# Kernel optimization log

Measured on AMD Instinct MI355X. Metric: run time of the kernel, lower is better.

Reference implementation:

```python
import jax, jax.numpy as jnp
import numpy as np

N = 100000   # nodes
E = 1600000  # edges
H = 128      # num_features == hidden_size
C = 64       # num_classes
BN_EPS = 1e-5


def setup_inputs() -> dict:
    key = jax.random.key(0)
    ks = jax.random.split(key, 11)
    return {
        "x": jax.random.normal(ks[0], (N, H), jnp.float32),
        "edge_index": jax.random.randint(ks[1], (2, E), 0, N, dtype=jnp.int32),
        "edge_attr": jax.random.normal(ks[2], (E,), jnp.float32),
        "conv_w": jax.random.normal(ks[3], (2, 3, H, H), jnp.float32) / np.sqrt(H).astype(np.float32),
        "conv_b": jax.random.normal(ks[4], (2, 3, H), jnp.float32) * 0.1,
        "bn_g": jax.random.uniform(ks[5], (2, 3, H), jnp.float32, 0.5, 1.5),
        "bn_b": jax.random.normal(ks[6], (2, 3, H), jnp.float32) * 0.1,
        "bn_m": jax.random.normal(ks[7], (2, 3, H), jnp.float32) * 0.1,
        "bn_v": jax.random.uniform(ks[8], (2, 3, H), jnp.float32, 0.5, 1.5),
        "fc_w": jax.random.normal(ks[9], (H, C), jnp.float32) / np.sqrt(H).astype(np.float32),
        "fc_b": jax.random.normal(ks[10], (C,), jnp.float32) * 0.1,
    }


def _gin_conv(h, edge_index, w, b, g, beta, m, v):
    # GIN: out = MLP((1+eps)*x + sum_{j in N(i)} x_j), eps=0 (PyG default)
    src, dst = edge_index[0], edge_index[1]
    agg = jax.ops.segment_sum(h[src], dst, num_segments=N)  # [N,H] scatter-add
    h = h + agg
    for i in range(3):  # Linear -> BatchNorm1d (eval stats) -> ReLU
        h = h @ w[i] + b[i]
        h = (h - m[i]) * jax.lax.rsqrt(v[i] + BN_EPS) * g[i] + beta[i]
        h = jax.nn.relu(h)
    return h


def reference(x, edge_index, edge_attr, conv_w, conv_b, bn_g, bn_b, bn_m, bn_v, fc_w, fc_b):
    # edge_attr is ignored by default PyG GINConv (no edge weighting in GIN)
    h = jax.nn.relu(_gin_conv(x, edge_index, conv_w[0], conv_b[0], bn_g[0], bn_b[0], bn_m[0], bn_v[0]))
    h = jax.nn.relu(_gin_conv(h, edge_index, conv_w[1], conv_b[1], bn_g[1], bn_b[1], bn_m[1], bn_v[1]))
    # dropout is identity in eval mode
    logits = h @ fc_w + fc_b  # [N,C]
    return jax.nn.log_softmax(logits, axis=1)
```

## Files before the change

### kernel.cpp

```cpp
#include <hip/hip_runtime.h>

#define NN 100000
#define NE 1600000
#define HF 128
#define NC 64
#define AP 136
#define NB 196
#define BSH 9
#define BMASK 511
#define BCAP 9216

typedef __bf16 bf16x8 __attribute__((ext_vector_type(8)));
typedef float  f32x4  __attribute__((ext_vector_type(4)));
typedef unsigned short us8 __attribute__((ext_vector_type(8)));

__device__ __forceinline__ unsigned short f2b(float x) {
  unsigned int u = __float_as_uint(x);
  u += 0x7FFFu + ((u >> 16) & 1u);
  return (unsigned short)(u >> 16);
}
__device__ __forceinline__ float b2f(unsigned short b) {
  return __uint_as_float(((unsigned int)b) << 16);
}

__global__ void prep_weights(const float* __restrict__ conv_w, const float* __restrict__ conv_b,
                             const float* __restrict__ bn_g, const float* __restrict__ bn_b,
                             const float* __restrict__ bn_m, const float* __restrict__ bn_v,
                             const float* __restrict__ fc_w,
                             unsigned short* __restrict__ wt, unsigned short* __restrict__ wtf,
                             float* __restrict__ sarr, float* __restrict__ tarr) {
  int idx = blockIdx.x * 256 + threadIdx.x;
  if (idx < 6 * HF * HF) {
    int j  = idx & 7;
    int m  = (idx >> 3) & 15;
    int q  = (idx >> 7) & 3;
    int nt = (idx >> 9) & 7;
    int k0 = (idx >> 12) & 3;
    int ls = idx >> 14;
    int k = k0 * 32 + q * 8 + j;
    int n = nt * 16 + m;
    wt[idx] = f2b(conv_w[(ls * HF + k) * HF + n]);
  }
  if (idx < HF * NC) {
    int j  = idx & 7;
    int m  = (idx >> 3) & 15;
    int q  = (idx >> 7) & 3;
    int nt = (idx >> 9) & 3;
    int k0 = idx >> 11;
    int k = k0 * 32 + q * 8 + j;
    int c = nt * 16 + m;
    wtf[idx] = f2b(fc_w[k * NC + c]);
  }
  if (idx < 6 * HF) {
    float s = bn_g[idx] * rsqrtf(bn_v[idx] + 1e-5f);
    sarr[idx] = s;
    tarr[idx] = (conv_b[idx] - bn_m[idx]) * s + bn_b[idx];
  }
}

__global__ __launch_bounds__(256) void cast_bf16(const float* __restrict__ x,
                                                 unsigned short* __restrict__ xb) {
  size_t i = (size_t)(blockIdx.x * 256 + threadIdx.x) * 8;
  float4 a = *(const float4*)(x + i);
  float4 b = *(const float4*)(x + i + 4);
  us8 v = { f2b(a.x), f2b(a.y), f2b(a.z), f2b(a.w),
            f2b(b.x), f2b(b.y), f2b(b.z), f2b(b.w) };
  *(us8*)(xb + i) = v;
}

__global__ void init_gcur(int* __restrict__ gcur) {
  int t = threadIdx.x;
  if (t < NB) gcur[t] = t * BCAP;
}

__global__ __launch_bounds__(256) void bin_edges(const int* __restrict__ src,
                                                 const int* __restrict__ dst,
                                                 int* __restrict__ gcur,
                                                 unsigned int* __restrict__ binned) {
  __shared__ int hist[NB];
  int t = threadIdx.x;
  if (t < NB) hist[t] = 0;
  __syncthreads();
  int base = blockIdx.x * 8192;
  for (int j = 0; j < 32; j++) {
    int e = base + j * 256 + t;
    if (e < NE) atomicAdd(&hist[dst[e] >> BSH], 1);
  }
  __syncthreads();
  if (t < NB) {
    int c = hist[t];
    if (c) hist[t] = atomicAdd(&gcur[t], c);
  }
  __syncthreads();
  for (int j = 0; j < 32; j++) {
    int e = base + j * 256 + t;
    if (e < NE) {
      int d = dst[e];
      int b = d >> BSH;
      int p = atomicAdd(&hist[b], 1);
      binned[p] = (unsigned int)src[e] | ((unsigned int)(d & BMASK) << 17);
    }
  }
}

__global__ __launch_bounds__(256) void build_csr(const unsigned int* __restrict__ binned,
                                                 const int* __restrict__ gcur,
                                                 int* __restrict__ offs,
                                                 int* __restrict__ deg,
                                                 int* __restrict__ csr) {
  __shared__ int ncnt[512];
  __shared__ int sm[256];
  int t = threadIdx.x;
  int b = blockIdx.x;
  int beg = b * BCAP;
  int cntb = gcur[b] - beg;
  ncnt[t] = 0; ncnt[t + 256] = 0;
  __syncthreads();
  for (int e = beg + t; e < beg + cntb; e += 256) atomicAdd(&ncnt[binned[e] >> 17], 1);
  __syncthreads();
  int c0 = ncnt[2 * t], c1 = ncnt[2 * t + 1];
  int s = c0 + c1;
  sm[t] = s; __syncthreads();
  for (int off = 1; off < 256; off <<= 1) {
    int u = (t >= off) ? sm[t - off] : 0;
    __syncthreads();
    sm[t] += u;
    __syncthreads();
  }
  int ex = sm[t] - s + beg;
  int node0 = (b << BSH) + 2 * t;
  if (node0 < NN)     { offs[node0]     = ex;      deg[node0]     = c0; }
  if (node0 + 1 < NN) { offs[node0 + 1] = ex + c0; deg[node0 + 1] = c1; }
  ncnt[2 * t]     = ex;
  ncnt[2 * t + 1] = ex + c0;
  __syncthreads();
  for (int e = beg + t; e < beg + cntb; e += 256) {
    unsigned int u = binned[e];
    int p = atomicAdd(&ncnt[u >> 17], 1);
    csr[p] = (int)(u & 0x1FFFFu);
  }
}

__global__ __launch_bounds__(256) void aggregate(const unsigned short* __restrict__ h,
                                                 const int* __restrict__ offs,
                                                 const int* __restrict__ deg,
                                                 const int* __restrict__ csr,
                                                 unsigned short* __restrict__ out) {
  int wave = threadIdx.x >> 6;
  int lane = threadIdx.x & 63;
  int node = blockIdx.x * 4 + wave;
  if (node >= NN) return;
  int g  = lane >> 4;
  int sl = lane & 15;
  int beg = offs[node];
  int dg  = deg[node];

  float acc[8];
  if (g == 0) {
    us8 v = *(const us8*)(h + (size_t)node * HF + sl * 8);
    #pragma unroll
    for (int i = 0; i < 8; i++) acc[i] = b2f(v[i]);
  } else {
    #pragma unroll
    for (int i = 0; i < 8; i++) acc[i] = 0.f;
  }

  for (int e = beg + g; e < beg + dg; e += 4) {
    int s = csr[e];
    us8 v = *(const us8*)(h + (size_t)s * HF + sl * 8);
    #pragma unroll
    for (int i = 0; i < 8; i++) acc[i] += b2f(v[i]);
  }

  #pragma unroll
  for (int i = 0; i < 8; i++) {
    acc[i] += __shfl_xor(acc[i], 16, 64);
    acc[i] += __shfl_xor(acc[i], 32, 64);
  }
  if (g == 0) {
    us8 r;
    #pragma unroll
    for (int i = 0; i < 8; i++) r[i] = f2b(acc[i]);
    *(us8*)(out + (size_t)node * HF + sl * 8) = r;
  }
}

__device__ __forceinline__ void mlp3_body(const unsigned short* __restrict__ in,
                                          unsigned short* Ab,
                                          const unsigned short* __restrict__ wt,
                                          const float* __restrict__ sarr,
                                          const float* __restrict__ tarr,
                                          int layer, int row0, int wave, int lane,
                                          bf16x8 af[4]) {
  int m = lane & 15, q = lane >> 4;
  int node = row0 + wave * 16 + m;
  int nclamp = (node < NN) ? node : 0;
  #pragma unroll
  for (int k0 = 0; k0 < 4; k0++)
    af[k0] = *(const bf16x8*)(in + (size_t)nclamp * HF + k0 * 32 + q * 8);

  const unsigned short* wbase = wt + layer * 3 * 16384;
  #pragma unroll
  for (int sub = 0; sub < 3; sub++) {
    const unsigned short* wsub = wbase + sub * 16384;
    f32x4 acc[8];
    #pragma unroll
    for (int nt = 0; nt < 8; nt++) {
      acc[nt] = (f32x4){0.f, 0.f, 0.f, 0.f};
      #pragma unroll
      for (int k0 = 0; k0 < 4; k0++) {
        bf16x8 bf = *(const bf16x8*)(wsub + ((k0 * 8 + nt) * 64 + lane) * 8);
        acc[nt] = __builtin_amdgcn_mfma_f32_16x16x32_bf16(af[k0], bf, acc[nt], 0, 0, 0);
      }
    }
    const float* sp = sarr + (layer * 3 + sub) * HF;
    const float* tp = tarr + (layer * 3 + sub) * HF;
    #pragma unroll
    for (int nt = 0; nt < 8; nt++) {
      int c = nt * 16 + m;
      float sc = sp[c], sh = tp[c];
      #pragma unroll
      for (int i = 0; i < 4; i++) {
        int r = wave * 16 + q * 4 + i;
        float y = fmaxf(acc[nt][i] * sc + sh, 0.f);
        Ab[r * AP + c] = f2b(y);
      }
    }
    #pragma unroll
    for (int k0 = 0; k0 < 4; k0++)
      af[k0] = *(const bf16x8*)&Ab[(wave * 16 + m) * AP + k0 * 32 + q * 8];
  }
}

__global__ __launch_bounds__(256) void mlp3(const unsigned short* __restrict__ in,
                                            unsigned short* __restrict__ out,
                                            const unsigned short* __restrict__ wt,
                                            const float* __restrict__ sarr,
                                            const float* __restrict__ tarr) {
  __shared__ unsigned short Ab[64 * AP];
  int t = threadIdx.x;
  int lane = t & 63, wave = t >> 6;
  int row0 = blockIdx.x * 64;
  bf16x8 af[4];
  mlp3_body(in, Ab, wt, sarr, tarr, 0, row0, wave, lane, af);

  for (int it = 0; it < 4; it++) {
    int idx = it * 64 + lane;
    int r = wave * 16 + (idx >> 4);
    int c = (idx & 15) << 3;
    int gr = row0 + r;
    if (gr < NN) *(us8*)(out + (size_t)gr * HF + c) = *(const us8*)&Ab[r * AP + c];
  }
}

__global__ __launch_bounds__(256) void mlp3fc(const unsigned short* __restrict__ in,
                                              float* __restrict__ out,
                                              const unsigned short* __restrict__ wt,
                                              const float* __restrict__ sarr,
                                              const float* __restrict__ tarr,
                                              const unsigned short* __restrict__ wtf,
                                              const float* __restrict__ fc_b) {
  __shared__ unsigned short Ab[64 * AP];
  int t = threadIdx.x;
  int lane = t & 63, wave = t >> 6;
  int row0 = blockIdx.x * 64;
  int m = lane & 15, q = lane >> 4;
  bf16x8 af[4];
  mlp3_body(in, Ab, wt, sarr, tarr, 1, row0, wave, lane, af);

  f32x4 acc[4];
  #pragma unroll
  for (int nt = 0; nt < 4; nt++) {
    acc[nt] = (f32x4){0.f, 0.f, 0.f, 0.f};
    #pragma unroll
    for (int k0 = 0; k0 < 4; k0++) {
      bf16x8 bf = *(const bf16x8*)(wtf + ((k0 * 4 + nt) * 64 + lane) * 8);
      acc[nt] = __builtin_amdgcn_mfma_f32_16x16x32_bf16(af[k0], bf, acc[nt], 0, 0, 0);
    }
  }
  float v[4][4];
  #pragma unroll
  for (int nt = 0; nt < 4; nt++) {
    float b = fc_b[nt * 16 + m];
    #pragma unroll
    for (int i = 0; i < 4; i++) v[nt][i] = acc[nt][i] + b;
  }
  float mx[4], sum[4];
  #pragma unroll
  for (int i = 0; i < 4; i++) {
    mx[i] = fmaxf(fmaxf(v[0][i], v[1][i]), fmaxf(v[2][i], v[3][i]));
    mx[i] = fmaxf(mx[i], __shfl_xor(mx[i], 1, 64));
    mx[i] = fmaxf(mx[i], __shfl_xor(mx[i], 2, 64));
    mx[i] = fmaxf(mx[i], __shfl_xor(mx[i], 4, 64));
    mx[i] = fmaxf(mx[i], __shfl_xor(mx[i], 8, 64));
    sum[i] = __expf(v[0][i] - mx[i]) + __expf(v[1][i] - mx[i])
           + __expf(v[2][i] - mx[i]) + __expf(v[3][i] - mx[i]);
    sum[i] += __shfl_xor(sum[i], 1, 64);
    sum[i] += __shfl_xor(sum[i], 2, 64);
    sum[i] += __shfl_xor(sum[i], 4, 64);
    sum[i] += __shfl_xor(sum[i], 8, 64);
    sum[i] = __logf(sum[i]) + mx[i];
  }
  #pragma unroll
  for (int i = 0; i < 4; i++) {
    int gr = row0 + wave * 16 + q * 4 + i;
    if (gr < NN) {
      #pragma unroll
      for (int nt = 0; nt < 4; nt++)
        out[(size_t)gr * NC + nt * 16 + m] = v[nt][i] - sum[i];
    }
  }
}

extern "C" void kernel_launch(void* const* d_in, const int* in_sizes, int n_in,
                              void* d_out, int out_size, void* d_ws, size_t ws_size,
                              hipStream_t stream) {
  const float* x      = (const float*)d_in[0];
  const int*   ei     = (const int*)d_in[1];
  const float* conv_w = (const float*)d_in[3];
  const float* conv_b = (const float*)d_in[4];
  const float* bn_g   = (const float*)d_in[5];
  const float* bn_b   = (const float*)d_in[6];
  const float* bn_m   = (const float*)d_in[7];
  const float* bn_v   = (const float*)d_in[8];
  const float* fc_w   = (const float*)d_in[9];
  const float* fc_b   = (const float*)d_in[10];
  float* out = (float*)d_out;

  const int* srcI = ei;
  const int* dstI = ei + NE;

  unsigned short* Xb   = (unsigned short*)d_ws;
  unsigned short* Abuf = Xb + (size_t)NN * HF;
  unsigned short* Bbuf = Abuf + (size_t)NN * HF;
  int* gcur   = (int*)(Bbuf + (size_t)NN * HF);
  int* offs   = gcur + 256;
  int* deg    = offs + 100004;
  unsigned int* binned = (unsigned int*)(deg + 100004);
  int* csr    = (int*)(binned + (size_t)NB * BCAP);
  unsigned short* wt  = (unsigned short*)(csr + (size_t)NB * BCAP);
  unsigned short* wtf = wt + 6 * HF * HF;
  float* sarr = (float*)(wtf + HF * NC);
  float* tarr = sarr + 6 * HF;

  prep_weights<<<384, 256, 0, stream>>>(conv_w, conv_b, bn_g, bn_b, bn_m, bn_v, fc_w,
                                        wt, wtf, sarr, tarr);
  cast_bf16<<<6250, 256, 0, stream>>>(x, Xb);
  init_gcur<<<1, 256, 0, stream>>>(gcur);
  bin_edges<<<196, 256, 0, stream>>>(srcI, dstI, gcur, binned);
  build_csr<<<196, 256, 0, stream>>>(binned, gcur, offs, deg, csr);

  aggregate<<<NN / 4, 256, 0, stream>>>(Xb, offs, deg, csr, Abuf);
  mlp3<<<(NN + 63) / 64, 256, 0, stream>>>(Abuf, Bbuf, wt, sarr, tarr);
  aggregate<<<NN / 4, 256, 0, stream>>>(Bbuf, offs, deg, csr, Abuf);
  mlp3fc<<<(NN + 63) / 64, 256, 0, stream>>>(Abuf, out, wt, sarr, tarr, wtf, fc_b);
}
```

Measured before the change: 383.3 us.

## Fuse prologue kernels and double edge-binning bucket count with wider blocks

Merges weight prep, input bf16 cast and bucket-cursor init into a single prologue kernel to cut launches. Halves the bucket width (256 nodes per bin, 391 bins) and uses 512-thread blocks for binning and CSR build so more workgroups run in parallel across the CUs. The binning kernel also keeps src/dst in registers between its two passes instead of reloading them. More bins mean more global atomics on the cursors, and bucket capacity headroom is tighter relative to the expected edges per bin.

```diff
diff --git a/kernel.cpp b/kernel.cpp
--- a/kernel.cpp
+++ b/kernel.cpp
@@ -5,10 +5,10 @@
 #define HF 128
 #define NC 64
 #define AP 136
-#define NB 196
-#define BSH 9
-#define BMASK 511
-#define BCAP 9216
+#define NB 391
+#define BSH 8
+#define BMASK 255
+#define BCAP 4608
 
 typedef __bf16 bf16x8 __attribute__((ext_vector_type(8)));
 typedef float  f32x4  __attribute__((ext_vector_type(4)));
@@ -23,13 +23,29 @@
   return __uint_as_float(((unsigned int)b) << 16);
 }
 
-__global__ void prep_weights(const float* __restrict__ conv_w, const float* __restrict__ conv_b,
-                             const float* __restrict__ bn_g, const float* __restrict__ bn_b,
-                             const float* __restrict__ bn_m, const float* __restrict__ bn_v,
-                             const float* __restrict__ fc_w,
-                             unsigned short* __restrict__ wt, unsigned short* __restrict__ wtf,
-                             float* __restrict__ sarr, float* __restrict__ tarr) {
+__global__ __launch_bounds__(256) void prologue(const float* __restrict__ x,
+                                                unsigned short* __restrict__ xb,
+                                                const float* __restrict__ conv_w,
+                                                const float* __restrict__ conv_b,
+                                                const float* __restrict__ bn_g,
+                                                const float* __restrict__ bn_b,
+                                                const float* __restrict__ bn_m,
+                                                const float* __restrict__ bn_v,
+                                                const float* __restrict__ fc_w,
+                                                unsigned short* __restrict__ wt,
+                                                unsigned short* __restrict__ wtf,
+                                                float* __restrict__ sarr,
+                                                float* __restrict__ tarr,
+                                                int* __restrict__ gcur) {
   int idx = blockIdx.x * 256 + threadIdx.x;
+  {
+    size_t i = (size_t)idx * 8;
+    float4 a = *(const float4*)(x + i);
+    float4 b = *(const float4*)(x + i + 4);
+    us8 v = { f2b(a.x), f2b(a.y), f2b(a.z), f2b(a.w),
+              f2b(b.x), f2b(b.y), f2b(b.z), f2b(b.w) };
+    *(us8*)(xb + i) = v;
+  }
   if (idx < 6 * HF * HF) {
     int j  = idx & 7;
     int m  = (idx >> 3) & 15;
@@ -56,24 +72,10 @@
     sarr[idx] = s;
     tarr[idx] = (conv_b[idx] - bn_m[idx]) * s + bn_b[idx];
   }
-}
-
-__global__ __launch_bounds__(256) void cast_bf16(const float* __restrict__ x,
-                                                 unsigned short* __restrict__ xb) {
-  size_t i = (size_t)(blockIdx.x * 256 + threadIdx.x) * 8;
-  float4 a = *(const float4*)(x + i);
-  float4 b = *(const float4*)(x + i + 4);
-  us8 v = { f2b(a.x), f2b(a.y), f2b(a.z), f2b(a.w),
-            f2b(b.x), f2b(b.y), f2b(b.z), f2b(b.w) };
-  *(us8*)(xb + i) = v;
-}
-
-__global__ void init_gcur(int* __restrict__ gcur) {
-  int t = threadIdx.x;
-  if (t < NB) gcur[t] = t * BCAP;
-}
-
-__global__ __launch_bounds__(256) void bin_edges(const int* __restrict__ src,
+  if (idx < NB) gcur[idx] = idx * BCAP;
+}
+
+__global__ __launch_bounds__(512) void bin_edges(const int* __restrict__ src,
                                                  const int* __restrict__ dst,
                                                  int* __restrict__ gcur,
                                                  unsigned int* __restrict__ binned) {
@@ -81,10 +83,15 @@
   int t = threadIdx.x;
   if (t < NB) hist[t] = 0;
   __syncthreads();
-  int base = blockIdx.x * 8192;
-  for (int j = 0; j < 32; j++) {
-    int e = base + j * 256 + t;
-    if (e < NE) atomicAdd(&hist[dst[e] >> BSH], 1);
+  int base = blockIdx.x * 4096;
+  int sv[8], dv[8];
+  #pragma unroll
+  for (int j = 0; j < 8; j++) {
+    int e = base + j * 512 + t;
+    bool ok = e < NE;
+    dv[j] = ok ? dst[e] : -1;
+    sv[j] = ok ? src[e] : 0;
+    if (ok) atomicAdd(&hist[dv[j] >> BSH], 1);
   }
   __syncthreads();
   if (t < NB) {
@@ -92,49 +99,48 @@
     if (c) hist[t] = atomicAdd(&gcur[t], c);
   }
   __syncthreads();
-  for (int j = 0; j < 32; j++) {
-    int e = base + j * 256 + t;
-    if (e < NE) {
-      int d = dst[e];
-      int b = d >> BSH;
+  #pragma unroll
+  for (int j = 0; j < 8; j++) {
+    if (dv[j] >= 0) {
+      int b = dv[j] >> BSH;
       int p = atomicAdd(&hist[b], 1);
-      binned[p] = (unsigned int)src[e] | ((unsigned int)(d & BMASK) << 17);
-    }
-  }
-}
-
-__global__ __launch_bounds__(256) void build_csr(const unsigned int* __restrict__ binned,
+      binned[p] = (unsigned int)sv[j] | ((unsigned int)(dv[j] & BMASK) << 17);
+    }
+  }
+}
+
+__global__ __launch_bounds__(512) void build_csr(const unsigned int* __restrict__ binned,
                                                  const int* __restrict__ gcur,
                                                  int* __restrict__ offs,
                                                  int* __restrict__ deg,
                                                  int* __restrict__ csr) {
-  __shared__ int ncnt[512];
+  __shared__ int ncnt[256];
   __shared__ int sm[256];
   int t = threadIdx.x;
   int b = blockIdx.x;
   int beg = b * BCAP;
   int cntb = gcur[b] - beg;
-  ncnt[t] = 0; ncnt[t + 256] = 0;
-  __syncthreads();
-  for (int e = beg + t; e < beg + cntb; e += 256) atomicAdd(&ncnt[binned[e] >> 17], 1);
-  __syncthreads();
-  int c0 = ncnt[2 * t], c1 = ncnt[2 * t + 1];
-  int s = c0 + c1;
-  sm[t] = s; __syncthreads();
+  if (t < 256) ncnt[t] = 0;
+  __syncthreads();
+  for (int e = beg + t; e < beg + cntb; e += 512) atomicAdd(&ncnt[binned[e] >> 17], 1);
+  __syncthreads();
+  int s = 0;
+  if (t < 256) { s = ncnt[t]; sm[t] = s; }
+  __syncthreads();
   for (int off = 1; off < 256; off <<= 1) {
-    int u = (t >= off) ? sm[t - off] : 0;
+    int u = (t < 256 && t >= off) ? sm[t - off] : 0;
     __syncthreads();
-    sm[t] += u;
+    if (t < 256) sm[t] += u;
     __syncthreads();
   }
-  int ex = sm[t] - s + beg;
-  int node0 = (b << BSH) + 2 * t;
-  if (node0 < NN)     { offs[node0]     = ex;      deg[node0]     = c0; }
-  if (node0 + 1 < NN) { offs[node0 + 1] = ex + c0; deg[node0 + 1] = c1; }
-  ncnt[2 * t]     = ex;
-  ncnt[2 * t + 1] = ex + c0;
-  __syncthreads();
-  for (int e = beg + t; e < beg + cntb; e += 256) {
+  if (t < 256) {
+    int ex = sm[t] - s + beg;
+    int node = (b << BSH) + t;
+    if (node < NN) { offs[node] = ex; deg[node] = s; }
+    ncnt[t] = ex;
+  }
+  __syncthreads();
+  for (int e = beg + t; e < beg + cntb; e += 512) {
     unsigned int u = binned[e];
     int p = atomicAdd(&ncnt[u >> 17], 1);
     csr[p] = (int)(u & 0x1FFFFu);
@@ -334,7 +340,7 @@
   unsigned short* Abuf = Xb + (size_t)NN * HF;
   unsigned short* Bbuf = Abuf + (size_t)NN * HF;
   int* gcur   = (int*)(Bbuf + (size_t)NN * HF);
-  int* offs   = gcur + 256;
+  int* offs   = gcur + 512;
   int* deg    = offs + 100004;
   unsigned int* binned = (unsigned int*)(deg + 100004);
   int* csr    = (int*)(binned + (size_t)NB * BCAP);
@@ -343,12 +349,10 @@
   float* sarr = (float*)(wtf + HF * NC);
   float* tarr = sarr + 6 * HF;
 
-  prep_weights<<<384, 256, 0, stream>>>(conv_w, conv_b, bn_g, bn_b, bn_m, bn_v, fc_w,
-                                        wt, wtf, sarr, tarr);
-  cast_bf16<<<6250, 256, 0, stream>>>(x, Xb);
-  init_gcur<<<1, 256, 0, stream>>>(gcur);
-  bin_edges<<<196, 256, 0, stream>>>(srcI, dstI, gcur, binned);
-  build_csr<<<196, 256, 0, stream>>>(binned, gcur, offs, deg, csr);
+  prologue<<<6250, 256, 0, stream>>>(x, Xb, conv_w, conv_b, bn_g, bn_b, bn_m, bn_v,
+                                     fc_w, wt, wtf, sarr, tarr, gcur);
+  bin_edges<<<NB, 512, 0, stream>>>(srcI, dstI, gcur, binned);
+  build_csr<<<NB, 512, 0, stream>>>(binned, gcur, offs, deg, csr);
 
   aggregate<<<NN / 4, 256, 0, stream>>>(Xb, offs, deg, csr, Abuf);
   mlp3<<<(NN + 63) / 64, 256, 0, stream>>>(Abuf, Bbuf, wt, sarr, tarr);
```

Result: faster. 343.2 us (-10.5%).
